# Kernel tuning notes

Measured on AMD Instinct MI355X. Metric: run time of the kernel, lower is better.

## Reference

```python
import jax, jax.numpy as jnp
import numpy as np

B, S, D = 2, 2048, 1024
H, DK, DV = 16, 64, 64


def setup_inputs() -> dict:
    key = jax.random.key(0)
    ks = jax.random.split(key, 9)
    s = 0.02
    return {
        "x": jax.random.normal(ks[0], (B, S, D), dtype=jnp.float32),
        "mask": jnp.zeros((B, S), dtype=bool),  # True = padded position
        "Wq": jax.random.normal(ks[1], (D, H * DK), dtype=jnp.float32) * s,
        "bq": jnp.zeros((H * DK,), dtype=jnp.float32),
        "Wk": jax.random.normal(ks[2], (D, H * DK), dtype=jnp.float32) * s,
        "bk": jnp.zeros((H * DK,), dtype=jnp.float32),
        "Wv": jax.random.normal(ks[3], (D, H * DV), dtype=jnp.float32) * s,
        "bv": jnp.zeros((H * DV,), dtype=jnp.float32),
        "Wo": jax.random.normal(ks[4], (H * DV, D), dtype=jnp.float32) * s,
        "bo": jnp.zeros((D,), dtype=jnp.float32),
    }


def reference(x, mask, Wq, bq, Wk, bk, Wv, bv, Wo, bo):
    Bx, Sx, _ = x.shape
    # projections -> [B, H, S, dk/dv]
    q = (x @ Wq + bq).reshape(Bx, Sx, H, DK).transpose(0, 2, 1, 3)
    k = (x @ Wk + bk).reshape(Bx, Sx, H, DK).transpose(0, 2, 1, 3)
    v = (x @ Wv + bv).reshape(Bx, Sx, H, DV).transpose(0, 2, 1, 3)
    # scaled QK^T: [B, H, Sq, Sk]
    scores = jnp.einsum("bhqd,bhkd->bhqk", q, k) / jnp.sqrt(jnp.float32(DK))
    neg_inf = jnp.float32(-jnp.inf)
    # padding mask: True masks out key positions
    scores = jnp.where(mask[:, None, None, :], neg_inf, scores)
    # causal mask
    causal = jnp.triu(jnp.ones((Sx, Sx), dtype=bool), k=1)
    scores = jnp.where(causal[None, None, :, :], neg_inf, scores)
    attn = jax.nn.softmax(scores, axis=-1)
    out = jnp.einsum("bhqk,bhkd->bhqd", attn, v)  # [B, H, S, dv]
    out = out.transpose(0, 2, 1, 3).reshape(Bx, Sx, H * DV)
    return out @ Wo + bo
```

## Files before the change

### kernel.cpp

```cpp
#include <hip/hip_runtime.h>
#include <stdint.h>

typedef __bf16 bf16_t;
typedef __bf16 bf16x8 __attribute__((ext_vector_type(8)));
typedef float f32x4 __attribute__((ext_vector_type(4)));

#define S_LEN 2048
#define D_MODEL 1024
#define NH 16
#define DKV 64
#define BATCH 2

#define QSCALE 0.1803368801111204f

__device__ __forceinline__ uint16_t f2bfu(float f) {
    union { float f; uint32_t u; } c; c.f = f;
    return (uint16_t)((c.u + 0x7fffu + ((c.u >> 16) & 1u)) >> 16);
}
__device__ __forceinline__ bf16_t f2bf(float f) {
    union { uint16_t s; bf16_t b; } o; o.s = f2bfu(f);
    return o.b;
}
__device__ __forceinline__ uint32_t pack2t(float lo, float hi) {
    union { float f; uint32_t u; } a, b; a.f = lo; b.f = hi;
    return __builtin_amdgcn_perm(b.u, a.u, 0x07060302);
}
__device__ __forceinline__ void gld_lds16(const bf16_t* g, bf16_t* l) {
    __builtin_amdgcn_global_load_lds(
        (const __attribute__((address_space(1))) void*)g,
        (__attribute__((address_space(3))) void*)l, 16, 0, 0);
}

__global__ __launch_bounds__(256) void k_convert_x(const float* __restrict__ x,
                                                   bf16_t* __restrict__ xb, int n) {
    int i = (blockIdx.x * 256 + threadIdx.x) * 4;
    if (i < n) {
        float4 v = *(const float4*)(x + i);
        xb[i + 0] = f2bf(v.x);
        xb[i + 1] = f2bf(v.y);
        xb[i + 2] = f2bf(v.z);
        xb[i + 3] = f2bf(v.w);
    }
}

__global__ __launch_bounds__(256) void k_transpose4(
    const float* __restrict__ Wq, const float* __restrict__ Wk,
    const float* __restrict__ Wv, const float* __restrict__ Wo,
    bf16_t* __restrict__ WqkvT, bf16_t* __restrict__ WoT) {
    __shared__ float tile[64][65];
    int k0 = blockIdx.x * 64;
    int n0 = blockIdx.y * 64;
    const float* W; bf16_t* WT; int np, nw;
    if (n0 < 3072) {
        W = (n0 < 1024) ? Wq : (n0 < 2048) ? Wk : Wv;
        np = n0 & 1023; WT = WqkvT; nw = n0;
    } else {
        W = Wo; np = n0 - 3072; WT = WoT; nw = n0 - 3072;
    }
    int tx = threadIdx.x & 63, ty = threadIdx.x >> 6;
    #pragma unroll
    for (int r = ty; r < 64; r += 4)
        tile[r][tx] = W[(size_t)(k0 + r) * 1024 + np + tx];
    __syncthreads();
    #pragma unroll
    for (int r = ty; r < 64; r += 4)
        WT[(size_t)(nw + r) * 1024 + k0 + tx] = f2bf(tile[tx][r]);
}

#define BM 128
#define BN 128
#define BKK 64

__global__ __launch_bounds__(256) void k_gemm_qkv(
    const bf16_t* __restrict__ A, const bf16_t* __restrict__ BT, int K,
    const float* __restrict__ bias0, const float* __restrict__ bias1,
    const float* __restrict__ bias2,
    bf16_t* __restrict__ outQ, bf16_t* __restrict__ outK, bf16_t* __restrict__ outVt) {
    __shared__ __align__(16) bf16_t As[BM * BKK];
    __shared__ __align__(16) bf16_t Bs[BN * BKK];
    int m0 = blockIdx.x * BM;
    int n0 = blockIdx.y * BN;
    int t = threadIdx.x;
    int wid = t >> 6, lane = t & 63, l15 = lane & 15, quad = lane >> 4;
    int wr = (wid >> 1) * 64, wc = (wid & 1) * 64;
    int srow = t >> 3;
    int schunk = (t & 7) ^ (srow & 7);
    int sldst = (t & 7) * 8;
    const f32x4 fzero = {0.f, 0.f, 0.f, 0.f};
    f32x4 acc[4][4];
    #pragma unroll
    for (int i = 0; i < 4; i++)
        #pragma unroll
        for (int j = 0; j < 4; j++) acc[i][j] = fzero;

    int r7 = l15 & 7;
    for (int k0 = 0; k0 < K; k0 += BKK) {
        #pragma unroll
        for (int p = 0; p < 4; p++) {
            int r = p * 32 + srow;
            gld_lds16(&A[(size_t)(m0 + r) * K + k0 + schunk * 8], &As[r * 64 + sldst]);
            gld_lds16(&BT[(size_t)(n0 + r) * K + k0 + schunk * 8], &Bs[r * 64 + sldst]);
        }
        __syncthreads();
        #pragma unroll
        for (int kk = 0; kk < BKK; kk += 32) {
            int g = quad + (kk >> 3);
            int col = ((g ^ r7) << 3);
            bf16x8 af[4], bfr[4];
            #pragma unroll
            for (int mt = 0; mt < 4; mt++)
                af[mt] = *(const bf16x8*)&As[(wr + mt * 16 + l15) * 64 + col];
            #pragma unroll
            for (int nt = 0; nt < 4; nt++)
                bfr[nt] = *(const bf16x8*)&Bs[(wc + nt * 16 + l15) * 64 + col];
            #pragma unroll
            for (int mt = 0; mt < 4; mt++)
                #pragma unroll
                for (int nt = 0; nt < 4; nt++)
                    acc[mt][nt] = __builtin_amdgcn_mfma_f32_16x16x32_bf16(
                        af[mt], bfr[nt], acc[mt][nt], 0, 0, 0);
        }
        __syncthreads();
    }

    #pragma unroll
    for (int mt = 0; mt < 4; mt++) {
        #pragma unroll
        for (int nt = 0; nt < 4; nt++) {
            int gc = n0 + wc + nt * 16 + l15;
            int sec = gc >> 10;
            int nn = gc & 1023;
            int h = nn >> 6, d = nn & 63;
            int gr0 = m0 + wr + mt * 16 + quad * 4;
            int b = gr0 >> 11, s0 = gr0 & 2047;
            if (sec == 2) {
                float bv = bias2[nn];
                uint2 pk;
                pk.x = pack2t(acc[mt][nt][0] + bv, acc[mt][nt][1] + bv);
                pk.y = pack2t(acc[mt][nt][2] + bv, acc[mt][nt][3] + bv);
                *(uint2*)&outVt[(((size_t)(b * NH + h)) * DKV + d) * S_LEN + s0] = pk;
            } else {
                const float* bias = (sec == 0) ? bias0 : bias1;
                float bv = bias[nn];
                #pragma unroll
                for (int r = 0; r < 4; r++) {
                    float val = acc[mt][nt][r] + bv;
                    size_t idx = (((size_t)(b * NH + h)) * S_LEN + s0 + r) * DKV + d;
                    if (sec == 0) outQ[idx] = f2bf(val * QSCALE);
                    else          outK[idx] = f2bf(val);
                }
            }
        }
    }
}

__global__ __launch_bounds__(256) void k_gemm_out(
    const bf16_t* __restrict__ A, const bf16_t* __restrict__ BT, int N, int K,
    const float* __restrict__ bias, float* __restrict__ outF) {
    __shared__ __align__(16) bf16_t As[128 * 64];
    __shared__ __align__(16) bf16_t Bs[64 * 64];
    int m0 = blockIdx.x * 128;
    int n0 = blockIdx.y * 64;
    int t = threadIdx.x;
    int wid = t >> 6, lane = t & 63, l15 = lane & 15, quad = lane >> 4;
    int wr = wid * 32;
    int srow = t >> 3;
    int schunk = (t & 7) ^ (srow & 7);
    int sldst = (t & 7) * 8;
    const f32x4 fzero = {0.f, 0.f, 0.f, 0.f};
    f32x4 acc[2][4];
    #pragma unroll
    for (int i = 0; i < 2; i++)
        #pragma unroll
        for (int j = 0; j < 4; j++) acc[i][j] = fzero;

    int r7 = l15 & 7;
    for (int k0 = 0; k0 < K; k0 += 64) {
        #pragma unroll
        for (int p = 0; p < 4; p++) {
            int r = p * 32 + srow;
            gld_lds16(&A[(size_t)(m0 + r) * K + k0 + schunk * 8], &As[r * 64 + sldst]);
        }
        #pragma unroll
        for (int p = 0; p < 2; p++) {
            int r = p * 32 + srow;
            gld_lds16(&BT[(size_t)(n0 + r) * K + k0 + schunk * 8], &Bs[r * 64 + sldst]);
        }
        __syncthreads();
        #pragma unroll
        for (int kk = 0; kk < 64; kk += 32) {
            int g = quad + (kk >> 3);
            int col = ((g ^ r7) << 3);
            bf16x8 af[2], bfr[4];
            #pragma unroll
            for (int mt = 0; mt < 2; mt++)
                af[mt] = *(const bf16x8*)&As[(wr + mt * 16 + l15) * 64 + col];
            #pragma unroll
            for (int nt = 0; nt < 4; nt++)
                bfr[nt] = *(const bf16x8*)&Bs[(nt * 16 + l15) * 64 + col];
            #pragma unroll
            for (int mt = 0; mt < 2; mt++)
                #pragma unroll
                for (int nt = 0; nt < 4; nt++)
                    acc[mt][nt] = __builtin_amdgcn_mfma_f32_16x16x32_bf16(
                        af[mt], bfr[nt], acc[mt][nt], 0, 0, 0);
        }
        __syncthreads();
    }

    #pragma unroll
    for (int mt = 0; mt < 2; mt++) {
        #pragma unroll
        for (int nt = 0; nt < 4; nt++) {
            #pragma unroll
            for (int r = 0; r < 4; r++) {
                int gr = m0 + wr + mt * 16 + quad * 4 + r;
                int gc = n0 + nt * 16 + l15;
                outF[(size_t)gr * N + gc] = acc[mt][nt][r] + bias[gc];
            }
        }
    }
}

__global__ __launch_bounds__(256) void k_attn8(
    const bf16_t* __restrict__ Q, const bf16_t* __restrict__ Kg,
    const bf16_t* __restrict__ Vt, const unsigned char* __restrict__ mask,
    bf16_t* __restrict__ O) {
    __shared__ __align__(16) bf16_t QPs[64 * 64];
    __shared__ __align__(16) bf16_t Ks[128 * 64];
    __shared__ __align__(16) bf16_t Vs[64 * 128];

    int bid = blockIdx.x;
    int bh = bid & 31;
    int u = bid >> 5;
    int a = u & 7, g2 = u >> 3;
    int qt = (g2 == 0) ? 31 - a : (g2 == 1) ? a : (g2 == 2) ? 23 - a : 8 + a;
    int b = bh >> 4, h = bh & 15;
    int t = threadIdx.x;
    int w = t >> 6, lane = t & 63, l15 = lane & 15, quad = lane >> 4;
    int r7 = l15 & 7;

    const bf16_t* Qbase = Q + ((size_t)bh * S_LEN + qt * 64) * DKV;
    {
        int r = t >> 3, c8 = t & 7;
        int sc = (c8 ^ (r & 7)) * 8;
        *(uint4*)&QPs[r * 64 + sc]        = *(const uint4*)&Qbase[(size_t)r * 64 + c8 * 8];
        *(uint4*)&QPs[(r + 32) * 64 + sc] = *(const uint4*)&Qbase[(size_t)(r + 32) * 64 + c8 * 8];
    }
    __syncthreads();
    bf16x8 qf0 = *(const bf16x8*)&QPs[(w * 16 + l15) * 64 + ((quad ^ r7) << 3)];
    bf16x8 qf1 = *(const bf16x8*)&QPs[(w * 16 + l15) * 64 + (((4 + quad) ^ r7) << 3)];

    const f32x4 fzero = {0.f, 0.f, 0.f, 0.f};
    f32x4 oacc[4];
    f32x4 lacc = fzero;
    #pragma unroll
    for (int nt = 0; nt < 4; nt++) oacc[nt] = fzero;

    const bf16_t one_b = (bf16_t)1.0f;
    const bf16x8 onesf = {one_b, one_b, one_b, one_b, one_b, one_b, one_b, one_b};

    int qg   = qt * 64 + w * 16 + l15;
    int qmin = qt * 64 + w * 16;
    int qmax = qmin + 15;
    int ktmax = qt >> 1;

    int srK = t >> 3;
    int scK = (t & 7) ^ (srK & 7);
    int slK = (t & 7) * 8;
    int srV = t >> 4;
    int scV = (t & 15) ^ (srV & 7);
    int slV = (t & 15) * 8;

    for (int kt = 0; kt <= ktmax; kt++) {
        __syncthreads();
        {
            const bf16_t* Kb = Kg + ((size_t)bh * S_LEN + kt * 128) * DKV;
            #pragma unroll
            for (int p = 0; p < 4; p++) {
                int r = p * 32 + srK;
                gld_lds16(&Kb[(size_t)r * 64 + scK * 8], &Ks[r * 64 + slK]);
            }
            #pragma unroll
            for (int p = 0; p < 4; p++) {
                int r = p * 16 + srV;
                gld_lds16(&Vt[((size_t)bh * DKV + r) * S_LEN + kt * 128 + scV * 8],
                          &Vs[r * 128 + slV]);
            }
        }
        __syncthreads();

        #pragma unroll
        for (int sub = 0; sub < 2; sub++) {
            int kbase = kt * 128 + sub * 64;
            if (kbase > qmax) break;

            uint32_t mb[4];
            #pragma unroll
            for (int mt = 0; mt < 4; mt++)
                mb[mt] = *(const uint32_t*)&mask[b * S_LEN + kbase + mt * 16 + quad * 4];

            f32x4 sacc[4];
            #pragma unroll
            for (int mt = 0; mt < 4; mt++) sacc[mt] = fzero;
            #pragma unroll
            for (int kk = 0; kk < 64; kk += 32) {
                bf16x8 qf = kk ? qf1 : qf0;
                int col = (((quad + (kk >> 3)) ^ r7) << 3);
                #pragma unroll
                for (int mt = 0; mt < 4; mt++) {
                    bf16x8 af = *(const bf16x8*)&Ks[(sub * 64 + mt * 16 + l15) * 64 + col];
                    sacc[mt] = __builtin_amdgcn_mfma_f32_16x16x32_bf16(af, qf, sacc[mt], 0, 0, 0);
                }
            }

            bool diag = (kbase + 63 > qmin);
            #pragma unroll
            for (int mt = 0; mt < 4; mt++) {
                #pragma unroll
                for (int r = 0; r < 4; r++)
                    sacc[mt][r] += (float)((mb[mt] >> (8 * r)) & 0xffu) * -1e30f;
                if (diag) {
                    int kgb = kbase + mt * 16 + quad * 4;
                    #pragma unroll
                    for (int r = 0; r < 4; r++)
                        if (kgb + r > qg) sacc[mt][r] = -1e30f;
                }
            }
            #pragma unroll
            for (int mt = 0; mt < 4; mt++) {
                uint2 pk;
                pk.x = pack2t(exp2f(sacc[mt][0]), exp2f(sacc[mt][1]));
                pk.y = pack2t(exp2f(sacc[mt][2]), exp2f(sacc[mt][3]));
                int pc = (mt * 2 + (quad >> 1)) ^ r7;
                *(uint2*)&QPs[(w * 16 + l15) * 64 + pc * 8 + (quad & 1) * 4] = pk;
            }

            #pragma unroll
            for (int kk = 0; kk < 64; kk += 32) {
                bf16x8 pf = *(const bf16x8*)&QPs[(w * 16 + l15) * 64 +
                                                 (((quad + (kk >> 3)) ^ r7) << 3)];
                int g2v = sub * 8 + (kk >> 3) + quad;
                int vcol = ((g2v ^ r7) << 3);
                #pragma unroll
                for (int nt = 0; nt < 4; nt++) {
                    bf16x8 vf = *(const bf16x8*)&Vs[(nt * 16 + l15) * 128 + vcol];
                    oacc[nt] = __builtin_amdgcn_mfma_f32_16x16x32_bf16(pf, vf, oacc[nt], 0, 0, 0);
                }
                lacc = __builtin_amdgcn_mfma_f32_16x16x32_bf16(pf, onesf, lacc, 0, 0, 0);
            }
        }
    }

    #pragma unroll
    for (int r = 0; r < 4; r++) {
        float l = lacc[r];
        float invl = l > 0.f ? 1.f / l : 0.f;
        int q = qt * 64 + w * 16 + quad * 4 + r;
        #pragma unroll
        for (int nt = 0; nt < 4; nt++) {
            int d = nt * 16 + l15;
            O[((size_t)b * S_LEN + q) * D_MODEL + h * DKV + d] = f2bf(oacc[nt][r] * invl);
        }
    }
}

extern "C" void kernel_launch(void* const* d_in, const int* in_sizes, int n_in,
                              void* d_out, int out_size, void* d_ws, size_t ws_size,
                              hipStream_t stream) {
    const float* x = (const float*)d_in[0];
    const unsigned char* mask = (const unsigned char*)d_in[1];
    const float* Wq = (const float*)d_in[2];
    const float* bq = (const float*)d_in[3];
    const float* Wk = (const float*)d_in[4];
    const float* bk = (const float*)d_in[5];
    const float* Wv = (const float*)d_in[6];
    const float* bv = (const float*)d_in[7];
    const float* Wo = (const float*)d_in[8];
    const float* bo = (const float*)d_in[9];
    float* out = (float*)d_out;

    char* ws = (char*)d_ws;
    const size_t MB = 1024 * 1024;
    bf16_t* xb    = (bf16_t*)(ws + 0 * MB);
    bf16_t* WqkvT = (bf16_t*)(ws + 8 * MB);
    bf16_t* WoT   = (bf16_t*)(ws + 14 * MB);
    bf16_t* Qb    = (bf16_t*)(ws + 16 * MB);
    bf16_t* Kb    = (bf16_t*)(ws + 24 * MB);
    bf16_t* Vtb   = (bf16_t*)(ws + 32 * MB);
    bf16_t* AOb   = (bf16_t*)(ws + 40 * MB);

    k_convert_x<<<dim3(4096), dim3(256), 0, stream>>>(x, xb, 4 * 1024 * 1024);
    k_transpose4<<<dim3(16, 64), dim3(256), 0, stream>>>(Wq, Wk, Wv, Wo, WqkvT, WoT);
    k_gemm_qkv<<<dim3(32, 24), dim3(256), 0, stream>>>(
        xb, WqkvT, 1024, bq, bk, bv, Qb, Kb, Vtb);
    k_attn8<<<dim3(1024), dim3(256), 0, stream>>>(Qb, Kb, Vtb, mask, AOb);
    k_gemm_out<<<dim3(32, 16), dim3(256), 0, stream>>>(
        AOb, WoT, 1024, 1024, bo, out);
}
```

Measured before the change: 190.8 us.

## Split long causal query tiles across two blocks and add combine kernel

```diff
diff --git a/kernel.cpp b/kernel.cpp
--- a/kernel.cpp
+++ b/kernel.cpp
@@ -222,10 +222,10 @@
     }
 }
 
-__global__ __launch_bounds__(256) void k_attn8(
+__global__ __launch_bounds__(256) void k_attn9(
     const bf16_t* __restrict__ Q, const bf16_t* __restrict__ Kg,
     const bf16_t* __restrict__ Vt, const unsigned char* __restrict__ mask,
-    bf16_t* __restrict__ O) {
+    bf16_t* __restrict__ Opart, float* __restrict__ lpart) {
     __shared__ __align__(16) bf16_t QPs[64 * 64];
     __shared__ __align__(16) bf16_t Ks[128 * 64];
     __shared__ __align__(16) bf16_t Vs[64 * 128];
@@ -233,9 +233,17 @@
     int bid = blockIdx.x;
     int bh = bid & 31;
     int u = bid >> 5;
-    int a = u & 7, g2 = u >> 3;
-    int qt = (g2 == 0) ? 31 - a : (g2 == 1) ? a : (g2 == 2) ? 23 - a : 8 + a;
-    int b = bh >> 4, h = bh & 15;
+    int qt, s;
+    if (u < 32) { qt = 16 + (u >> 1); s = u & 1; }
+    else        { qt = 47 - u;        s = 0; }
+    int nkt = (qt >> 1) + 1;
+    int h1 = (nkt + 1) >> 1;
+    int k0i = (qt >= 16 && s == 1) ? h1 : 0;
+    int kni = (qt >= 16 && s == 0) ? h1 : nkt;
+    int slot = (qt < 16) ? qt : 16 + ((qt - 16) << 1) + s;
+    int pidx = bh * 48 + slot;
+
+    int b = bh >> 4;
     int t = threadIdx.x;
     int w = t >> 6, lane = t & 63, l15 = lane & 15, quad = lane >> 4;
     int r7 = l15 & 7;
@@ -263,7 +271,6 @@
     int qg   = qt * 64 + w * 16 + l15;
     int qmin = qt * 64 + w * 16;
     int qmax = qmin + 15;
-    int ktmax = qt >> 1;
 
     int srK = t >> 3;
     int scK = (t & 7) ^ (srK & 7);
@@ -272,7 +279,7 @@
     int scV = (t & 15) ^ (srV & 7);
     int slV = (t & 15) * 8;
 
-    for (int kt = 0; kt <= ktmax; kt++) {
+    for (int kt = k0i; kt < kni; kt++) {
         __syncthreads();
         {
             const bf16_t* Kb = Kg + ((size_t)bh * S_LEN + kt * 128) * DKV;
@@ -352,17 +359,58 @@
         }
     }
 
-    #pragma unroll
-    for (int r = 0; r < 4; r++) {
-        float l = lacc[r];
-        float invl = l > 0.f ? 1.f / l : 0.f;
-        int q = qt * 64 + w * 16 + quad * 4 + r;
-        #pragma unroll
-        for (int nt = 0; nt < 4; nt++) {
-            int d = nt * 16 + l15;
-            O[((size_t)b * S_LEN + q) * D_MODEL + h * DKV + d] = f2bf(oacc[nt][r] * invl);
-        }
-    }
+    int prow = w * 16 + quad * 4;
+    bf16_t* Op = Opart + (size_t)pidx * 4096;
+    #pragma unroll
+    for (int r = 0; r < 4; r++)
+        #pragma unroll
+        for (int nt = 0; nt < 4; nt++)
+            Op[(prow + r) * 64 + nt * 16 + l15] = f2bf(oacc[nt][r]);
+    if (l15 == 0) {
+        #pragma unroll
+        for (int r = 0; r < 4; r++)
+            lpart[(size_t)pidx * 64 + prow + r] = lacc[r];
+    }
+}
+
+__global__ __launch_bounds__(256) void k_combine(
+    const bf16_t* __restrict__ Opart, const float* __restrict__ lpart,
+    bf16_t* __restrict__ AO) {
+    __shared__ float linv[64];
+    int qt = blockIdx.x, bh = blockIdx.y;
+    int b = bh >> 4, h = bh & 15;
+    int nsp = (qt < 16) ? 1 : 2;
+    int slot0 = (qt < 16) ? qt : 16 + ((qt - 16) << 1);
+    size_t p0 = (size_t)(bh * 48 + slot0);
+    int t = threadIdx.x;
+    if (t < 64) {
+        float l = lpart[p0 * 64 + t];
+        if (nsp == 2) l += lpart[(p0 + 1) * 64 + t];
+        linv[t] = (l > 0.f) ? 1.f / l : 0.f;
+    }
+    __syncthreads();
+    int row = t >> 2, c0 = (t & 3) * 16;
+    const uint16_t* s0p = (const uint16_t*)Opart + p0 * 4096 + row * 64 + c0;
+    float v[16];
+    #pragma unroll
+    for (int j = 0; j < 16; j++) {
+        union { uint32_t u; float f; } cv; cv.u = (uint32_t)s0p[j] << 16;
+        v[j] = cv.f;
+    }
+    if (nsp == 2) {
+        #pragma unroll
+        for (int j = 0; j < 16; j++) {
+            union { uint32_t u; float f; } cv; cv.u = (uint32_t)s0p[4096 + j] << 16;
+            v[j] += cv.f;
+        }
+    }
+    float invl = linv[row];
+    union { uint16_t sv[16]; uint4 u[2]; } pk;
+    #pragma unroll
+    for (int j = 0; j < 16; j++) pk.sv[j] = f2bfu(v[j] * invl);
+    bf16_t* dst = AO + ((size_t)b * S_LEN + qt * 64 + row) * D_MODEL + h * DKV + c0;
+    *(uint4*)dst = pk.u[0];
+    *(uint4*)(dst + 8) = pk.u[1];
 }
 
 extern "C" void kernel_launch(void* const* d_in, const int* in_sizes, int n_in,
@@ -383,6 +431,8 @@
     char* ws = (char*)d_ws;
     const size_t MB = 1024 * 1024;
     bf16_t* xb    = (bf16_t*)(ws + 0 * MB);
+    bf16_t* Opart = (bf16_t*)(ws + 0 * MB);
+    float*  lpart = (float*) (ws + 13 * MB);
     bf16_t* WqkvT = (bf16_t*)(ws + 8 * MB);
     bf16_t* WoT   = (bf16_t*)(ws + 14 * MB);
     bf16_t* Qb    = (bf16_t*)(ws + 16 * MB);
@@ -394,7 +444,8 @@
     k_transpose4<<<dim3(16, 64), dim3(256), 0, stream>>>(Wq, Wk, Wv, Wo, WqkvT, WoT);
     k_gemm_qkv<<<dim3(32, 24), dim3(256), 0, stream>>>(
         xb, WqkvT, 1024, bq, bk, bv, Qb, Kb, Vtb);
-    k_attn8<<<dim3(1024), dim3(256), 0, stream>>>(Qb, Kb, Vtb, mask, AOb);
+    k_attn9<<<dim3(1536), dim3(256), 0, stream>>>(Qb, Kb, Vtb, mask, Opart, lpart);
+    k_combine<<<dim3(32, 32), dim3(256), 0, stream>>>(Opart, lpart, AOb);
     k_gemm_out<<<dim3(32, 16), dim3(256), 0, stream>>>(
         AOb, WoT, 1024, 1024, bo, out);
 }
```

New measurement: 193.7 us. No clear change (+1.5%).
